# Kernel optimization log

Measured on AMD Instinct MI355X. Metric: run time of the kernel, lower is better.

Reference implementation:

```python
import jax, jax.numpy as jnp
import numpy as np

D_MODEL = 256
N_LAYER = 16
VOCAB = 24
D_INNER = 512
D_STATE = 16
D_CONV = 4
DT_RANK = 16
B = 2
L = 2048
EPS = 1e-5


def setup_inputs() -> dict:
    key = jax.random.key(0)
    ks = jax.random.split(key, 10)
    f = lambda k, shape, s=0.02: jax.random.normal(k, shape, dtype=jnp.float32) * s
    # S4D-real style A init: A_log = log(1..d_state), broadcast over channels/layers
    a_log = jnp.tile(jnp.log(jnp.arange(1, D_STATE + 1, dtype=jnp.float32)), (N_LAYER, D_INNER, 1))
    return {
        'input_ids': jax.random.randint(ks[0], (B, L), 0, VOCAB),
        'embedding': f(ks[1], (VOCAB, D_MODEL)),
        'in_proj_w': f(ks[2], (N_LAYER, 2 * D_INNER, D_MODEL)),
        'conv_w': f(ks[3], (N_LAYER, D_INNER, D_CONV), 0.1),
        'conv_b': jnp.zeros((N_LAYER, D_INNER), dtype=jnp.float32),
        'x_proj_w': f(ks[4], (N_LAYER, DT_RANK + 2 * D_STATE, D_INNER)),
        'dt_proj_w': f(ks[5], (N_LAYER, D_INNER, DT_RANK), 0.1),
        'dt_proj_b': jnp.full((N_LAYER, D_INNER), -4.6, dtype=jnp.float32),  # softplus(-4.6) ~ 0.01 = dt_init floor
        'A_log': a_log,
        'D': jnp.ones((N_LAYER, D_INNER), dtype=jnp.float32),
        'out_proj_w': f(ks[6], (N_LAYER, D_MODEL, D_INNER), 0.005),
        'norm_w': jnp.ones((N_LAYER, D_MODEL), dtype=jnp.float32),
        'norm_f_w': jnp.ones((D_MODEL,), dtype=jnp.float32),
        'lm_head_w': f(ks[7], (20, D_MODEL)),
    }


def _rmsnorm(x, w, eps=EPS):
    return x * jax.lax.rsqrt(jnp.mean(x * x, axis=-1, keepdims=True) + eps) * w


def _selective_scan(dA, dBx, C):
    # dA, dBx: (B, L, d_inner, d_state); C: (B, L, d_state)
    # h_t = dA_t * h_{t-1} + dBx_t  (parallel associative scan over L)
    def comb(left, right):
        a_l, b_l = left
        a_r, b_r = right
        return a_l * a_r, a_r * b_l + b_r
    _, hs = jax.lax.associative_scan(comb, (dA, dBx), axis=1)
    return jnp.einsum('blds,bls->bld', hs, C)


def _mamba(h, in_w, cw, cb, xw, dtw, dtb, a_log, d_skip, ow):
    # h: (B, L, d_model)
    xz = jnp.einsum('bld,ed->ble', h, in_w)            # (B, L, 2*d_inner)
    x, z = jnp.split(xz, 2, axis=-1)
    # depthwise causal conv1d over L
    xt = jnp.transpose(x, (0, 2, 1))                   # (B, d_inner, L)
    xc = jax.lax.conv_general_dilated(
        xt, cw[:, None, :], window_strides=(1,), padding=[(D_CONV - 1, 0)],
        feature_group_count=D_INNER)
    x = jax.nn.silu(jnp.transpose(xc, (0, 2, 1)) + cb)  # (B, L, d_inner)
    dbc = jnp.einsum('bld,ed->ble', x, xw)             # (B, L, dt_rank+2*d_state)
    dt, Bm, Cm = jnp.split(dbc, [DT_RANK, DT_RANK + D_STATE], axis=-1)
    dt = jax.nn.softplus(jnp.einsum('blr,dr->bld', dt, dtw) + dtb)  # (B, L, d_inner)
    A = -jnp.exp(a_log)                                # (d_inner, d_state)
    dA = jnp.exp(dt[..., None] * A)                    # (B, L, d_inner, d_state)
    dBx = dt[..., None] * Bm[:, :, None, :] * x[..., None]
    y = _selective_scan(dA, dBx, Cm) + d_skip * x
    y = y * jax.nn.silu(z)
    return jnp.einsum('bld,ed->ble', y, ow)


def reference(input_ids, embedding, in_proj_w, conv_w, conv_b, x_proj_w,
              dt_proj_w, dt_proj_b, A_log, D, out_proj_w, norm_w, norm_f_w,
              lm_head_w):
    h = embedding[input_ids]                           # (B, L, d_model)
    residual = None
    for i in range(N_LAYER):
        residual = h + residual if residual is not None else h
        hn = _rmsnorm(residual, norm_w[i])
        h = _mamba(hn, in_proj_w[i], conv_w[i], conv_b[i], x_proj_w[i],
                   dt_proj_w[i], dt_proj_b[i], A_log[i], D[i], out_proj_w[i])
    residual = h + residual
    h = _rmsnorm(residual, norm_f_w)
    return jnp.einsum('bld,vd->blv', h, lm_head_w)     # (B, L, 20)
```

## Files before the change

kernel.cpp:

```cpp
#include <hip/hip_runtime.h>
#include <hip/hip_bf16.h>

#define D_MODEL 256
#define N_LAYER 16
#define VOCAB 24
#define D_INNER 512
#define D_STATE 16
#define D_CONV 4
#define DT_RANK 16
#define BATCH 2
#define SEQ 2048
#define NTOK (BATCH*SEQ)
#define EPS 1e-5f
#define NC 128
#define CL (SEQ/NC)
#define NSC (BATCH*D_INNER*D_STATE)

typedef __hip_bfloat16 bf16;
typedef __attribute__((ext_vector_type(8))) short short8;
typedef __attribute__((ext_vector_type(4))) float f32x4;

__device__ __forceinline__ float silu(float v) { return v / (1.f + __expf(-v)); }
__device__ __forceinline__ float bf2f(bf16 v) { return __bfloat162float(v); }
__device__ __forceinline__ float bfs2f(short s) {
    return __uint_as_float(((unsigned)(unsigned short)s) << 16);
}
__device__ __forceinline__ short bfr(float x) {
    unsigned u = __float_as_uint(x);
    return (short)((u + 0x7fffu + ((u >> 16) & 1u)) >> 16);
}

__global__ void k_wcvt_all(const float* __restrict__ in_w, const float* __restrict__ out_w,
                           const float* __restrict__ x_w, short* __restrict__ in_wb,
                           short* __restrict__ out_wb, short* __restrict__ x_wb) {
    int idx = blockIdx.x * 256 + threadIdx.x;
    if (idx < 4194304) {
        in_wb[idx] = bfr(in_w[idx]);
    } else if (idx < 4194304 + 2097152) {
        int j = idx - 4194304;
        out_wb[j] = bfr(out_w[j]);
    } else {
        int j = idx - 4194304 - 2097152;
        x_wb[j] = bfr(x_w[j]);
    }
}

__global__ void k_embed(const int* __restrict__ ids, const float* __restrict__ emb,
                        float* __restrict__ residual, float* __restrict__ nsum) {
    __shared__ float wred[4];
    int tok = blockIdx.x, c = threadIdx.x;
    float v = emb[ids[tok] * D_MODEL + c];
    residual[tok * 256 + c] = v;
    float s = v * v;
    #pragma unroll
    for (int off = 32; off >= 1; off >>= 1) s += __shfl_xor(s, off);
    if ((c & 63) == 0) wred[c >> 6] = s;
    __syncthreads();
    if (c == 0) {
        float tot = wred[0] + wred[1] + wred[2] + wred[3];
        *(float4*)(nsum + (size_t)tok * 4) = make_float4(tot, 0.f, 0.f, 0.f);
    }
}

__global__ void k_rmsnorm(const float* __restrict__ residual, const float* __restrict__ w,
                          bf16* __restrict__ hn) {
    __shared__ float wred[4];
    int tok = blockIdx.x, c = threadIdx.x;
    float v = residual[tok * 256 + c];
    float s = v * v;
    #pragma unroll
    for (int off = 32; off >= 1; off >>= 1) s += __shfl_xor(s, off);
    if ((c & 63) == 0) wred[c >> 6] = s;
    __syncthreads();
    float tot = wred[0] + wred[1] + wred[2] + wred[3];
    float scale = rsqrtf(tot * (1.f / 256.f) + EPS);
    hn[tok * 256 + c] = __float2bfloat16(v * scale * w[c]);
}

__global__ __launch_bounds__(256) void k_gemm1_mfma(const float* __restrict__ Rres,
                                                    const float* __restrict__ nsum,
                                                    const float* __restrict__ nw,
                                                    const short* __restrict__ W16,
                                                    bf16* __restrict__ xh,
                                                    bf16* __restrict__ zb) {
    __shared__ short AsL[64 * 40];
    __shared__ short WsL[128 * 40];
    const int bm = blockIdx.x * 64, bn = blockIdx.y * 128;
    const int tid = threadIdx.x;
    const int wave = tid >> 6, lane = tid & 63;
    const int wm = (wave & 1) * 32, wn = (wave >> 1) * 32;
    const int quad = lane >> 4, lr = lane & 15;
    const int srow = tid >> 2, skq = (tid & 3) * 8;
    const float4 ns = *(const float4*)(nsum + (size_t)(bm + srow) * 4);
    const float scale = rsqrtf((ns.x + ns.y + ns.z + ns.w) * (1.f / 256.f) + EPS);
    f32x4 acc[2][2][2] = {};
    for (int k0 = 0; k0 < 256; k0 += 32) {
        float av[8], wv[8];
        *(float4*)&av[0] = *(const float4*)(Rres + (size_t)(bm + srow) * 256 + k0 + skq);
        *(float4*)&av[4] = *(const float4*)(Rres + (size_t)(bm + srow) * 256 + k0 + skq + 4);
        *(float4*)&wv[0] = *(const float4*)(nw + k0 + skq);
        *(float4*)&wv[4] = *(const float4*)(nw + k0 + skq + 4);
        short8 a8;
        #pragma unroll
        for (int j = 0; j < 8; j++) a8[j] = bfr(av[j] * scale * wv[j]);
        short8 w8[2];
        w8[0] = *(const short8*)(W16 + (size_t)(bn + srow) * 256 + k0 + skq);
        w8[1] = *(const short8*)(W16 + (size_t)(bn + 64 + srow) * 256 + k0 + skq);
        __syncthreads();
        *(short8*)&AsL[srow * 40 + skq] = a8;
        *(short8*)&WsL[srow * 40 + skq] = w8[0];
        *(short8*)&WsL[(64 + srow) * 40 + skq] = w8[1];
        __syncthreads();
        short8 af[2], bf[2][2];
        #pragma unroll
        for (int i = 0; i < 2; i++)
            af[i] = *(const short8*)&AsL[(wm + i * 16 + lr) * 40 + quad * 8];
        #pragma unroll
        for (int nb = 0; nb < 2; nb++)
            #pragma unroll
            for (int i = 0; i < 2; i++)
                bf[nb][i] = *(const short8*)&WsL[(nb * 64 + wn + i * 16 + lr) * 40 + quad * 8];
        #pragma unroll
        for (int nb = 0; nb < 2; nb++)
            #pragma unroll
            for (int mi = 0; mi < 2; mi++)
                #pragma unroll
                for (int ni = 0; ni < 2; ni++)
                    acc[nb][mi][ni] = __builtin_amdgcn_mfma_f32_16x16x32_bf16(
                        af[mi], bf[nb][ni], acc[nb][mi][ni], 0, 0, 0);
    }
    #pragma unroll
    for (int nb = 0; nb < 2; nb++) {
        #pragma unroll
        for (int mi = 0; mi < 2; mi++) {
            #pragma unroll
            for (int ni = 0; ni < 2; ni++) {
                int gcol = bn + nb * 64 + wn + ni * 16 + lr;
                #pragma unroll
                for (int r = 0; r < 4; r++) {
                    int grow = bm + wm + mi * 16 + quad * 4 + r;
                    float v = acc[nb][mi][ni][r];
                    if (gcol < 512) xh[(size_t)grow * 512 + gcol] = __float2bfloat16(v);
                    else            zb[(size_t)grow * 512 + gcol - 512] = __float2bfloat16(v);
                }
            }
        }
    }
}

__global__ __launch_bounds__(256) void k_gemm2_mfma(const bf16* __restrict__ Abf,
                                                    const short* __restrict__ W16,
                                                    float* __restrict__ residual,
                                                    float* __restrict__ nsum) {
    __shared__ short AsL[64 * 40];
    __shared__ short WsL[64 * 40];
    __shared__ float rsum[64][2];
    const short* A16 = (const short*)Abf;
    const int bm = blockIdx.x * 64, bn = blockIdx.y * 64;
    const int tid = threadIdx.x;
    const int wave = tid >> 6, lane = tid & 63;
    const int wm = (wave & 1) * 32, wn = (wave >> 1) * 32;
    const int quad = lane >> 4, lr = lane & 15;
    const int srow = tid >> 2, skq = (tid & 3) * 8;
    f32x4 acc[2][2] = {};
    for (int k0 = 0; k0 < 512; k0 += 32) {
        short8 a8 = *(const short8*)(A16 + (size_t)(bm + srow) * 512 + k0 + skq);
        short8 w8 = *(const short8*)(W16 + (size_t)(bn + srow) * 512 + k0 + skq);
        __syncthreads();
        *(short8*)&AsL[srow * 40 + skq] = a8;
        *(short8*)&WsL[srow * 40 + skq] = w8;
        __syncthreads();
        short8 af[2], bf[2];
        #pragma unroll
        for (int i = 0; i < 2; i++) {
            af[i] = *(const short8*)&AsL[(wm + i * 16 + lr) * 40 + quad * 8];
            bf[i] = *(const short8*)&WsL[(wn + i * 16 + lr) * 40 + quad * 8];
        }
        #pragma unroll
        for (int mi = 0; mi < 2; mi++)
            #pragma unroll
            for (int ni = 0; ni < 2; ni++)
                acc[mi][ni] = __builtin_amdgcn_mfma_f32_16x16x32_bf16(
                    af[mi], bf[ni], acc[mi][ni], 0, 0, 0);
    }
    float sq[2][4] = {};
    #pragma unroll
    for (int mi = 0; mi < 2; mi++) {
        #pragma unroll
        for (int ni = 0; ni < 2; ni++) {
            int gcol = bn + wn + ni * 16 + lr;
            #pragma unroll
            for (int r = 0; r < 4; r++) {
                int grow = bm + wm + mi * 16 + quad * 4 + r;
                size_t idx = (size_t)grow * 256 + gcol;
                float v = residual[idx] + acc[mi][ni][r];
                residual[idx] = v;
                sq[mi][r] += v * v;
            }
        }
    }
    #pragma unroll
    for (int off = 1; off < 16; off <<= 1) {
        #pragma unroll
        for (int mi = 0; mi < 2; mi++)
            #pragma unroll
            for (int r = 0; r < 4; r++)
                sq[mi][r] += __shfl_xor(sq[mi][r], off);
    }
    if (lr == 0) {
        #pragma unroll
        for (int mi = 0; mi < 2; mi++)
            #pragma unroll
            for (int r = 0; r < 4; r++)
                rsum[wm + mi * 16 + quad * 4 + r][wave >> 1] = sq[mi][r];
    }
    __syncthreads();
    if (tid < 64)
        nsum[(size_t)(bm + tid) * 4 + blockIdx.y] = rsum[tid][0] + rsum[tid][1];
}

__global__ __launch_bounds__(256) void k_convxproj(const bf16* __restrict__ xh,
                                                   const float* __restrict__ cw,
                                                   const float* __restrict__ cb,
                                                   const short* __restrict__ W16,
                                                   bf16* __restrict__ xb,
                                                   float* __restrict__ dbc) {
    __shared__ short Cs[16][520];
    const int bm = blockIdx.x * 16;
    const int tid = threadIdx.x;
    const int wave = tid >> 6, lane = tid & 63;
    const int quad = lane >> 4, lr = lane & 15;
    const int wn = wave * 16;

    short8 wreg[16];
    if (wn < 48) {
        const short* wp = W16 + (size_t)(wn + lr) * 512 + quad * 8;
        #pragma unroll
        for (int k = 0; k < 16; k++) wreg[k] = *(const short8*)(wp + k * 32);
    }

    {
        const int d8 = (tid & 63) * 8;
        const int rg = (tid >> 6) * 4;
        const int lbase = (bm & 2047) + rg;
        const int gbase = bm + rg;
        float xv[7][8];
        #pragma unroll
        for (int i = 0; i < 7; i++) {
            int l = lbase - 3 + i;
            if (l >= 0) {
                short8 r8 = *(const short8*)((const short*)xh +
                               (size_t)(gbase - 3 + i) * 512 + d8);
                #pragma unroll
                for (int j = 0; j < 8; j++) xv[i][j] = bfs2f(r8[j]);
            } else {
                #pragma unroll
                for (int j = 0; j < 8; j++) xv[i][j] = 0.f;
            }
        }
        float cwv[8][4], cbv[8];
        #pragma unroll
        for (int j = 0; j < 8; j++) {
            *(float4*)&cwv[j][0] = *(const float4*)(cw + (d8 + j) * 4);
            cbv[j] = cb[d8 + j];
        }
        #pragma unroll
        for (int t = 0; t < 4; t++) {
            short8 o;
            #pragma unroll
            for (int j = 0; j < 8; j++) {
                float acc = cbv[j] + xv[t][j] * cwv[j][0] + xv[t+1][j] * cwv[j][1]
                                   + xv[t+2][j] * cwv[j][2] + xv[t+3][j] * cwv[j][3];
                o[j] = bfr(silu(acc));
            }
            *(short8*)&Cs[rg + t][d8] = o;
            *(short8*)((short*)xb + (size_t)(gbase + t) * 512 + d8) = o;
        }
    }
    __syncthreads();

    if (wn < 48) {
        f32x4 acc = {};
        #pragma unroll
        for (int k = 0; k < 16; k++) {
            short8 af = *(const short8*)&Cs[lr][k * 32 + quad * 8];
            acc = __builtin_amdgcn_mfma_f32_16x16x32_bf16(af, wreg[k], acc, 0, 0, 0);
        }
        int gcol = wn + lr;
        #pragma unroll
        for (int r = 0; r < 4; r++)
            dbc[(size_t)(bm + quad * 4 + r) * 48 + gcol] = acc[r];
    }
}

__global__ __launch_bounds__(64) void k_scanA(const bf16* __restrict__ xb,
                                              const float* __restrict__ dbc,
                                              const float* __restrict__ dtw,
                                              const float* __restrict__ dtb,
                                              const float* __restrict__ a_log,
                                              float* __restrict__ Aprod,
                                              float* __restrict__ Hfin) {
    int gid = blockIdx.x * 64 + threadIdx.x;
    int bd = gid & 1023;
    int c = gid >> 10;
    int d = bd & 511, b = bd >> 9;
    float A[16], h[16], ap[16], wdt[16];
    #pragma unroll
    for (int q = 0; q < 4; q++)
        *(float4*)&wdt[q*4] = *(const float4*)(dtw + d * 16 + q * 4);
    #pragma unroll
    for (int s = 0; s < 16; s++) {
        A[s] = -__expf(a_log[d * 16 + s]);
        h[s] = 0.f; ap[s] = 1.f;
    }
    float bdt = dtb[d];
    int tok0 = b * SEQ + c * CL;
    const bf16* xp = xb + (size_t)tok0 * 512 + d;
    const float* rp = dbc + (size_t)tok0 * 48;
    for (int t = 0; t < CL; t++) {
        float rv[32];
        #pragma unroll
        for (int q = 0; q < 8; q++) *(float4*)&rv[q*4] = *(const float4*)(rp + t * 48 + q * 4);
        float dtr = bdt;
        #pragma unroll
        for (int r = 0; r < 16; r++) dtr = fmaf(rv[r], wdt[r], dtr);
        float dtv = (dtr > 20.f) ? dtr : __logf(1.f + __expf(dtr));
        float u = dtv * bf2f(xp[t * 512]);
        #pragma unroll
        for (int s = 0; s < 16; s++) {
            float dA = __expf(dtv * A[s]);
            h[s] = fmaf(dA, h[s], u * rv[16 + s]);
            ap[s] *= dA;
        }
    }
    float* Ap = Aprod + (size_t)c * NSC + bd * 16;
    float* Hp = Hfin  + (size_t)c * NSC + bd * 16;
    #pragma unroll
    for (int q = 0; q < 4; q++) {
        *(float4*)(Ap + q * 4) = make_float4(ap[q*4], ap[q*4+1], ap[q*4+2], ap[q*4+3]);
        *(float4*)(Hp + q * 4) = make_float4(h[q*4], h[q*4+1], h[q*4+2], h[q*4+3]);
    }
}

__global__ __launch_bounds__(64) void k_scanB(const float* __restrict__ Aprod,
                                              float* __restrict__ Hfin) {
    int chain = blockIdx.x * 64 + threadIdx.x;
    float h = 0.f;
    for (int cg = 0; cg < NC; cg += 16) {
        float a[16], f[16];
        #pragma unroll
        for (int j = 0; j < 16; j++) {
            size_t i = (size_t)(cg + j) * NSC + chain;
            a[j] = Aprod[i];
            f[j] = Hfin[i];
        }
        #pragma unroll
        for (int j = 0; j < 16; j++) {
            size_t i = (size_t)(cg + j) * NSC + chain;
            Hfin[i] = h;
            h = fmaf(a[j], h, f[j]);
        }
    }
}

__global__ __launch_bounds__(64) void k_scanC(const bf16* __restrict__ xb,
                                              const bf16* __restrict__ zb,
                                              const float* __restrict__ dbc,
                                              const float* __restrict__ dtw,
                                              const float* __restrict__ dtb,
                                              const float* __restrict__ a_log,
                                              const float* __restrict__ Dp,
                                              const float* __restrict__ Hstart,
                                              bf16* __restrict__ yb) {
    int gid = blockIdx.x * 64 + threadIdx.x;
    int bd = gid & 1023;
    int c = gid >> 10;
    int d = bd & 511, b = bd >> 9;
    float A[16], h[16], wdt[16];
    const float* Hp = Hstart + (size_t)c * NSC + bd * 16;
    #pragma unroll
    for (int q = 0; q < 4; q++)
        *(float4*)&wdt[q*4] = *(const float4*)(dtw + d * 16 + q * 4);
    #pragma unroll
    for (int s = 0; s < 16; s++) {
        A[s] = -__expf(a_log[d * 16 + s]);
        h[s] = Hp[s];
    }
    float bdt = dtb[d];
    float Dv = Dp[d];
    int tok0 = b * SEQ + c * CL;
    const bf16* xp = xb + (size_t)tok0 * 512 + d;
    const bf16* zp = zb + (size_t)tok0 * 512 + d;
    const float* rp = dbc + (size_t)tok0 * 48;
    bf16* yp = yb + (size_t)tok0 * 512 + d;
    for (int t = 0; t < CL; t++) {
        float rv[48];
        #pragma unroll
        for (int q = 0; q < 12; q++) *(float4*)&rv[q*4] = *(const float4*)(rp + t * 48 + q * 4);
        float dtr = bdt;
        #pragma unroll
        for (int r = 0; r < 16; r++) dtr = fmaf(rv[r], wdt[r], dtr);
        float dtv = (dtr > 20.f) ? dtr : __logf(1.f + __expf(dtr));
        float xv = bf2f(xp[t * 512]);
        float u = dtv * xv;
        float sum = 0.f;
        #pragma unroll
        for (int s = 0; s < 16; s++) {
            float dA = __expf(dtv * A[s]);
            h[s] = fmaf(dA, h[s], u * rv[16 + s]);
            sum = fmaf(h[s], rv[32 + s], sum);
        }
        float zv = bf2f(zp[t * 512]);
        yp[t * 512] = __float2bfloat16((sum + Dv * xv) * silu(zv));
    }
}

__global__ void k_head(const bf16* __restrict__ hn, const float* __restrict__ lw,
                       float* __restrict__ out) {
    int idx = blockIdx.x * 256 + threadIdx.x;
    int tok = idx / 20, v = idx % 20;
    const short* a = (const short*)(hn + (size_t)tok * 256);
    const float* w = lw + (size_t)v * 256;
    float acc = 0.f;
    for (int k = 0; k < 256; k += 8) {
        short8 a8 = *(const short8*)(a + k);
        #pragma unroll
        for (int j = 0; j < 8; j++) acc = fmaf(bfs2f(a8[j]), w[k + j], acc);
    }
    out[idx] = acc;
}

extern "C" void kernel_launch(void* const* d_in, const int* in_sizes, int n_in,
                              void* d_out, int out_size, void* d_ws, size_t ws_size,
                              hipStream_t stream) {
    const int*   ids    = (const int*)d_in[0];
    const float* emb    = (const float*)d_in[1];
    const float* in_w   = (const float*)d_in[2];
    const float* conv_w = (const float*)d_in[3];
    const float* conv_b = (const float*)d_in[4];
    const float* x_w    = (const float*)d_in[5];
    const float* dt_w   = (const float*)d_in[6];
    const float* dt_b   = (const float*)d_in[7];
    const float* a_log  = (const float*)d_in[8];
    const float* d_skip = (const float*)d_in[9];
    const float* out_w  = (const float*)d_in[10];
    const float* norm_w = (const float*)d_in[11];
    const float* norm_f = (const float*)d_in[12];
    const float* lm_w   = (const float*)d_in[13];
    float* out = (float*)d_out;

    char* ws = (char*)d_ws;
    float* residual = (float*)(ws + 0);
    bf16*  hn       = (bf16*) (ws + 4194304);
    bf16*  xh       = (bf16*) (ws + 6291456);
    bf16*  zb       = (bf16*) (ws + 10485760);
    bf16*  xb       = (bf16*) (ws + 14680064);
    float* dbc      = (float*)(ws + 18874368);
    float* Aprod    = (float*)(ws + 23855104);
    float* Hfin     = (float*)(ws + 32243712);
    short* in_wb    = (short*)(ws + 40632320);
    short* out_wb   = (short*)(ws + 49020928);
    short* x_wb     = (short*)(ws + 53215232);
    float* nsum     = (float*)(ws + 54001664);
    bf16*  yb       = xh;

    k_wcvt_all<<<6684672 / 256, 256, 0, stream>>>(in_w, out_w, x_w, in_wb, out_wb, x_wb);
    k_embed<<<NTOK, 256, 0, stream>>>(ids, emb, residual, nsum);

    for (int i = 0; i < N_LAYER; i++) {
        dim3 g1(NTOK / 64, 1024 / 128);
        k_gemm1_mfma<<<g1, 256, 0, stream>>>(residual, nsum, norm_w + i * D_MODEL,
                                             in_wb + (size_t)i * 262144, xh, zb);
        k_convxproj<<<NTOK / 16, 256, 0, stream>>>(
            xh, conv_w + (size_t)i * 512 * 4, conv_b + (size_t)i * 512,
            x_wb + (size_t)i * 24576, xb, dbc);
        k_scanA<<<(1024 * NC) / 64, 64, 0, stream>>>(
            xb, dbc, dt_w + (size_t)i * 512 * 16, dt_b + (size_t)i * 512,
            a_log + (size_t)i * 512 * 16, Aprod, Hfin);
        k_scanB<<<NSC / 64, 64, 0, stream>>>(Aprod, Hfin);
        k_scanC<<<(1024 * NC) / 64, 64, 0, stream>>>(
            xb, zb, dbc, dt_w + (size_t)i * 512 * 16, dt_b + (size_t)i * 512,
            a_log + (size_t)i * 512 * 16, d_skip + (size_t)i * 512, Hfin, yb);
        dim3 g2(NTOK / 64, 256 / 64);
        k_gemm2_mfma<<<g2, 256, 0, stream>>>(yb, out_wb + (size_t)i * 131072,
                                             residual, nsum);
    }

    k_rmsnorm<<<NTOK, 256, 0, stream>>>(residual, norm_f, hn);
    k_head<<<320, 256, 0, stream>>>(hn, lm_w, out);
}
```

Measured before the change: 1.339 ms.

## Fuse chunk scan pass into conv/x_proj kernel and merge init and head kernels

Folds the first pass of the chunked selective scan into the conv+x_proj kernel. Each 16-token block already holds the conv output and dt/B projections in shared memory, so it computes per-chunk state and decay products from LDS instead of rereading them from global memory. It also merges weight conversion with embedding into one launch, and final RMSNorm with the LM head into one kernel. This removes launches and global round trips, but each block's scan part now runs 2 channels per thread over 16 serial steps, which could lengthen the fused kernel and lower its parallelism.

```diff
diff --git a/kernel.cpp b/kernel.cpp
--- a/kernel.cpp
+++ b/kernel.cpp
@@ -15,6 +15,7 @@
 #define NC 128
 #define CL (SEQ/NC)
 #define NSC (BATCH*D_INNER*D_STATE)
+#define WCVT_BLOCKS 26112
 
 typedef __hip_bfloat16 bf16;
 typedef __attribute__((ext_vector_type(8))) short short8;
@@ -30,51 +31,37 @@
     return (short)((u + 0x7fffu + ((u >> 16) & 1u)) >> 16);
 }
 
-__global__ void k_wcvt_all(const float* __restrict__ in_w, const float* __restrict__ out_w,
-                           const float* __restrict__ x_w, short* __restrict__ in_wb,
-                           short* __restrict__ out_wb, short* __restrict__ x_wb) {
-    int idx = blockIdx.x * 256 + threadIdx.x;
-    if (idx < 4194304) {
-        in_wb[idx] = bfr(in_w[idx]);
-    } else if (idx < 4194304 + 2097152) {
-        int j = idx - 4194304;
-        out_wb[j] = bfr(out_w[j]);
+__global__ void k_init(const float* __restrict__ in_w, const float* __restrict__ out_w,
+                       const float* __restrict__ x_w, short* __restrict__ in_wb,
+                       short* __restrict__ out_wb, short* __restrict__ x_wb,
+                       const int* __restrict__ ids, const float* __restrict__ emb,
+                       float* __restrict__ residual, float* __restrict__ nsum) {
+    __shared__ float wred[4];
+    if (blockIdx.x < WCVT_BLOCKS) {
+        int idx = blockIdx.x * 256 + threadIdx.x;
+        if (idx < 4194304) {
+            in_wb[idx] = bfr(in_w[idx]);
+        } else if (idx < 4194304 + 2097152) {
+            int j = idx - 4194304;
+            out_wb[j] = bfr(out_w[j]);
+        } else {
+            int j = idx - 4194304 - 2097152;
+            x_wb[j] = bfr(x_w[j]);
+        }
     } else {
-        int j = idx - 4194304 - 2097152;
-        x_wb[j] = bfr(x_w[j]);
-    }
-}
-
-__global__ void k_embed(const int* __restrict__ ids, const float* __restrict__ emb,
-                        float* __restrict__ residual, float* __restrict__ nsum) {
-    __shared__ float wred[4];
-    int tok = blockIdx.x, c = threadIdx.x;
-    float v = emb[ids[tok] * D_MODEL + c];
-    residual[tok * 256 + c] = v;
-    float s = v * v;
-    #pragma unroll
-    for (int off = 32; off >= 1; off >>= 1) s += __shfl_xor(s, off);
-    if ((c & 63) == 0) wred[c >> 6] = s;
-    __syncthreads();
-    if (c == 0) {
-        float tot = wred[0] + wred[1] + wred[2] + wred[3];
-        *(float4*)(nsum + (size_t)tok * 4) = make_float4(tot, 0.f, 0.f, 0.f);
-    }
-}
-
-__global__ void k_rmsnorm(const float* __restrict__ residual, const float* __restrict__ w,
-                          bf16* __restrict__ hn) {
-    __shared__ float wred[4];
-    int tok = blockIdx.x, c = threadIdx.x;
-    float v = residual[tok * 256 + c];
-    float s = v * v;
-    #pragma unroll
-    for (int off = 32; off >= 1; off >>= 1) s += __shfl_xor(s, off);
-    if ((c & 63) == 0) wred[c >> 6] = s;
-    __syncthreads();
-    float tot = wred[0] + wred[1] + wred[2] + wred[3];
-    float scale = rsqrtf(tot * (1.f / 256.f) + EPS);
-    hn[tok * 256 + c] = __float2bfloat16(v * scale * w[c]);
+        int tok = blockIdx.x - WCVT_BLOCKS, c = threadIdx.x;
+        float v = emb[ids[tok] * D_MODEL + c];
+        residual[tok * 256 + c] = v;
+        float s = v * v;
+        #pragma unroll
+        for (int off = 32; off >= 1; off >>= 1) s += __shfl_xor(s, off);
+        if ((c & 63) == 0) wred[c >> 6] = s;
+        __syncthreads();
+        if (c == 0) {
+            float tot = wred[0] + wred[1] + wred[2] + wred[3];
+            *(float4*)(nsum + (size_t)tok * 4) = make_float4(tot, 0.f, 0.f, 0.f);
+        }
+    }
 }
 
 __global__ __launch_bounds__(256) void k_gemm1_mfma(const float* __restrict__ Rres,
@@ -219,13 +206,19 @@
         nsum[(size_t)(bm + tid) * 4 + blockIdx.y] = rsum[tid][0] + rsum[tid][1];
 }
 
-__global__ __launch_bounds__(256) void k_convxproj(const bf16* __restrict__ xh,
-                                                   const float* __restrict__ cw,
-                                                   const float* __restrict__ cb,
-                                                   const short* __restrict__ W16,
-                                                   bf16* __restrict__ xb,
-                                                   float* __restrict__ dbc) {
+__global__ __launch_bounds__(256) void k_cxs(const bf16* __restrict__ xh,
+                                             const float* __restrict__ cw,
+                                             const float* __restrict__ cb,
+                                             const short* __restrict__ W16,
+                                             const float* __restrict__ dtw,
+                                             const float* __restrict__ dtb,
+                                             const float* __restrict__ a_log,
+                                             bf16* __restrict__ xb,
+                                             float* __restrict__ dbc,
+                                             float* __restrict__ Aprod,
+                                             float* __restrict__ Hfin) {
     __shared__ short Cs[16][520];
+    __shared__ float Ds[16][52];
     const int bm = blockIdx.x * 16;
     const int tid = threadIdx.x;
     const int wave = tid >> 6, lane = tid & 63;
@@ -288,57 +281,67 @@
         }
         int gcol = wn + lr;
         #pragma unroll
-        for (int r = 0; r < 4; r++)
-            dbc[(size_t)(bm + quad * 4 + r) * 48 + gcol] = acc[r];
-    }
-}
-
-__global__ __launch_bounds__(64) void k_scanA(const bf16* __restrict__ xb,
-                                              const float* __restrict__ dbc,
-                                              const float* __restrict__ dtw,
-                                              const float* __restrict__ dtb,
-                                              const float* __restrict__ a_log,
-                                              float* __restrict__ Aprod,
-                                              float* __restrict__ Hfin) {
-    int gid = blockIdx.x * 64 + threadIdx.x;
-    int bd = gid & 1023;
-    int c = gid >> 10;
-    int d = bd & 511, b = bd >> 9;
-    float A[16], h[16], ap[16], wdt[16];
-    #pragma unroll
-    for (int q = 0; q < 4; q++)
-        *(float4*)&wdt[q*4] = *(const float4*)(dtw + d * 16 + q * 4);
-    #pragma unroll
-    for (int s = 0; s < 16; s++) {
-        A[s] = -__expf(a_log[d * 16 + s]);
-        h[s] = 0.f; ap[s] = 1.f;
-    }
-    float bdt = dtb[d];
-    int tok0 = b * SEQ + c * CL;
-    const bf16* xp = xb + (size_t)tok0 * 512 + d;
-    const float* rp = dbc + (size_t)tok0 * 48;
-    for (int t = 0; t < CL; t++) {
-        float rv[32];
-        #pragma unroll
-        for (int q = 0; q < 8; q++) *(float4*)&rv[q*4] = *(const float4*)(rp + t * 48 + q * 4);
-        float dtr = bdt;
-        #pragma unroll
-        for (int r = 0; r < 16; r++) dtr = fmaf(rv[r], wdt[r], dtr);
-        float dtv = (dtr > 20.f) ? dtr : __logf(1.f + __expf(dtr));
-        float u = dtv * bf2f(xp[t * 512]);
-        #pragma unroll
-        for (int s = 0; s < 16; s++) {
-            float dA = __expf(dtv * A[s]);
-            h[s] = fmaf(dA, h[s], u * rv[16 + s]);
-            ap[s] *= dA;
-        }
-    }
-    float* Ap = Aprod + (size_t)c * NSC + bd * 16;
-    float* Hp = Hfin  + (size_t)c * NSC + bd * 16;
-    #pragma unroll
-    for (int q = 0; q < 4; q++) {
-        *(float4*)(Ap + q * 4) = make_float4(ap[q*4], ap[q*4+1], ap[q*4+2], ap[q*4+3]);
-        *(float4*)(Hp + q * 4) = make_float4(h[q*4], h[q*4+1], h[q*4+2], h[q*4+3]);
+        for (int r = 0; r < 4; r++) {
+            float v = acc[r];
+            dbc[(size_t)(bm + quad * 4 + r) * 48 + gcol] = v;
+            Ds[quad * 4 + r][gcol] = v;
+        }
+    }
+    __syncthreads();
+
+    {
+        const int b = bm >> 11;
+        const int c = (bm & 2047) >> 4;
+        float A[2][16], h[2][16], ap[2][16], wdt[2][16], bdt[2];
+        #pragma unroll
+        for (int ch = 0; ch < 2; ch++) {
+            int d = tid + ch * 256;
+            #pragma unroll
+            for (int q = 0; q < 4; q++)
+                *(float4*)&wdt[ch][q*4] = *(const float4*)(dtw + d * 16 + q * 4);
+            #pragma unroll
+            for (int s = 0; s < 16; s++) {
+                A[ch][s] = -__expf(a_log[d * 16 + s]);
+                h[ch][s] = 0.f; ap[ch][s] = 1.f;
+            }
+            bdt[ch] = dtb[d];
+        }
+        for (int t = 0; t < CL; t++) {
+            float dtc[16], Bc[16];
+            #pragma unroll
+            for (int r = 0; r < 16; r++) dtc[r] = Ds[t][r];
+            #pragma unroll
+            for (int s = 0; s < 16; s++) Bc[s] = Ds[t][16 + s];
+            #pragma unroll
+            for (int ch = 0; ch < 2; ch++) {
+                int d = tid + ch * 256;
+                float dtr = bdt[ch];
+                #pragma unroll
+                for (int r = 0; r < 16; r++) dtr = fmaf(dtc[r], wdt[ch][r], dtr);
+                float dtv = (dtr > 20.f) ? dtr : __logf(1.f + __expf(dtr));
+                float u = dtv * bfs2f(((const short*)&Cs[t][0])[d]);
+                #pragma unroll
+                for (int s = 0; s < 16; s++) {
+                    float dA = __expf(dtv * A[ch][s]);
+                    h[ch][s] = fmaf(dA, h[ch][s], u * Bc[s]);
+                    ap[ch][s] *= dA;
+                }
+            }
+        }
+        #pragma unroll
+        for (int ch = 0; ch < 2; ch++) {
+            int d = tid + ch * 256;
+            int bd = b * 512 + d;
+            float* Ap = Aprod + (size_t)c * NSC + (size_t)bd * 16;
+            float* Hp = Hfin  + (size_t)c * NSC + (size_t)bd * 16;
+            #pragma unroll
+            for (int q = 0; q < 4; q++) {
+                *(float4*)(Ap + q * 4) = make_float4(ap[ch][q*4], ap[ch][q*4+1],
+                                                     ap[ch][q*4+2], ap[ch][q*4+3]);
+                *(float4*)(Hp + q * 4) = make_float4(h[ch][q*4], h[ch][q*4+1],
+                                                     h[ch][q*4+2], h[ch][q*4+3]);
+            }
+        }
     }
 }
 
@@ -415,19 +418,32 @@
     }
 }
 
-__global__ void k_head(const bf16* __restrict__ hn, const float* __restrict__ lw,
-                       float* __restrict__ out) {
-    int idx = blockIdx.x * 256 + threadIdx.x;
-    int tok = idx / 20, v = idx % 20;
-    const short* a = (const short*)(hn + (size_t)tok * 256);
-    const float* w = lw + (size_t)v * 256;
-    float acc = 0.f;
-    for (int k = 0; k < 256; k += 8) {
-        short8 a8 = *(const short8*)(a + k);
-        #pragma unroll
-        for (int j = 0; j < 8; j++) acc = fmaf(bfs2f(a8[j]), w[k + j], acc);
-    }
-    out[idx] = acc;
+__global__ void k_rmshead(const float* __restrict__ residual, const float* __restrict__ w,
+                          const float* __restrict__ lw, float* __restrict__ out) {
+    __shared__ float wred[4];
+    __shared__ float hrow[256];
+    int tok = blockIdx.x, c = threadIdx.x;
+    float v = residual[tok * 256 + c];
+    float s = v * v;
+    #pragma unroll
+    for (int off = 32; off >= 1; off >>= 1) s += __shfl_xor(s, off);
+    if ((c & 63) == 0) wred[c >> 6] = s;
+    __syncthreads();
+    float tot = wred[0] + wred[1] + wred[2] + wred[3];
+    float scale = rsqrtf(tot * (1.f / 256.f) + EPS);
+    hrow[c] = bfs2f(bfr(v * scale * w[c]));
+    __syncthreads();
+    int wave = c >> 6, lane = c & 63;
+    float4 hl = *(const float4*)&hrow[lane * 4];
+    #pragma unroll
+    for (int j = 0; j < 5; j++) {
+        int vv = wave * 5 + j;
+        float4 wl = *(const float4*)(lw + (size_t)vv * 256 + lane * 4);
+        float p = hl.x * wl.x + hl.y * wl.y + hl.z * wl.z + hl.w * wl.w;
+        #pragma unroll
+        for (int off = 32; off >= 1; off >>= 1) p += __shfl_xor(p, off);
+        if (lane == 0) out[(size_t)tok * 20 + vv] = p;
+    }
 }
 
 extern "C" void kernel_launch(void* const* d_in, const int* in_sizes, int n_in,
@@ -451,7 +467,6 @@
 
     char* ws = (char*)d_ws;
     float* residual = (float*)(ws + 0);
-    bf16*  hn       = (bf16*) (ws + 4194304);
     bf16*  xh       = (bf16*) (ws + 6291456);
     bf16*  zb       = (bf16*) (ws + 10485760);
     bf16*  xb       = (bf16*) (ws + 14680064);
@@ -464,19 +479,18 @@
     float* nsum     = (float*)(ws + 54001664);
     bf16*  yb       = xh;
 
-    k_wcvt_all<<<6684672 / 256, 256, 0, stream>>>(in_w, out_w, x_w, in_wb, out_wb, x_wb);
-    k_embed<<<NTOK, 256, 0, stream>>>(ids, emb, residual, nsum);
+    k_init<<<WCVT_BLOCKS + NTOK, 256, 0, stream>>>(in_w, out_w, x_w, in_wb, out_wb,
+                                                   x_wb, ids, emb, residual, nsum);
 
     for (int i = 0; i < N_LAYER; i++) {
         dim3 g1(NTOK / 64, 1024 / 128);
         k_gemm1_mfma<<<g1, 256, 0, stream>>>(residual, nsum, norm_w + i * D_MODEL,
                                              in_wb + (size_t)i * 262144, xh, zb);
-        k_convxproj<<<NTOK / 16, 256, 0, stream>>>(
+        k_cxs<<<NTOK / 16, 256, 0, stream>>>(
             xh, conv_w + (size_t)i * 512 * 4, conv_b + (size_t)i * 512,
-            x_wb + (size_t)i * 24576, xb, dbc);
-        k_scanA<<<(1024 * NC) / 64, 64, 0, stream>>>(
-            xb, dbc, dt_w + (size_t)i * 512 * 16, dt_b + (size_t)i * 512,
-            a_log + (size_t)i * 512 * 16, Aprod, Hfin);
+            x_wb + (size_t)i * 24576, dt_w + (size_t)i * 512 * 16,
+            dt_b + (size_t)i * 512, a_log + (size_t)i * 512 * 16,
+            xb, dbc, Aprod, Hfin);
         k_scanB<<<NSC / 64, 64, 0, stream>>>(Aprod, Hfin);
         k_scanC<<<(1024 * NC) / 64, 64, 0, stream>>>(
             xb, zb, dbc, dt_w + (size_t)i * 512 * 16, dt_b + (size_t)i * 512,
@@ -486,6 +500,5 @@
                                              residual, nsum);
     }
 
-    k_rmsnorm<<<NTOK, 256, 0, stream>>>(residual, norm_f, hn);
-    k_head<<<320, 256, 0, stream>>>(hn, lm_w, out);
-}
+    k_rmshead<<<NTOK, 256, 0, stream>>>(residual, norm_f, lm_w, out);
+}
```

Measured after the change: 1.216 ms. 1.1x faster.
